# Performance work log

Measured on AMD Instinct MI355X. Metric: run time of the kernel, lower is better.

Reference implementation:

```python
import jax, jax.numpy as jnp
import numpy as np

N = 50000
E = 400000
D = 256            # in_dim == out_dim for every branch
H = 8              # mulhead
DH = D // H        # 32
L = 2              # num_layer per branch
NUM_CLASS = 7
SUM_OUT = 5 * D    # classifier in_dim = 1280
EPS = 1e-9         # BatchNorm eps


def _bn(x):
    # BatchNorm1d training-mode forward (biased var), affine at init (gamma=1, beta=0)
    mu = jnp.mean(x, axis=0)
    var = jnp.var(x, axis=0)
    return (x - mu) / jnp.sqrt(var + EPS)


def _gat_layer(f, Ws, bs, Wn, bn_, a_s, a_n, row, col, vals):
    # f: [N, D]; Ws/Wn: [H, D, DH]; bs/bn_: [H, DH]; a_s/a_n: [H, DH]
    f_self = jax.nn.relu(jnp.einsum('nd,hdk->nhk', f, Ws) + bs)      # [N,H,DH]
    f_neigh = jax.nn.relu(jnp.einsum('nd,hdk->nhk', f, Wn) + bn_)    # [N,H,DH]
    att_s = jax.nn.leaky_relu(jnp.einsum('nhk,hk->nh', f_self, a_s), 0.2)  # [N,H]
    # NOTE: original code computes attention_neigh from f_self (faithful)
    att_n = jax.nn.leaky_relu(jnp.einsum('nhk,hk->nh', f_self, a_n), 0.2)  # [N,H]
    e_att = (att_s[row] + att_n[col]) * vals[:, None]                # [E,H]
    msg = e_att[:, :, None] * f_neigh[col]                           # [E,H,DH]
    out = jax.ops.segment_sum(msg, row, num_segments=N)              # [N,H,DH]
    return out.reshape(N, H * DH)                                    # head concat


def _gat(f, Ws, bs, Wn, bn_, a_s, a_n, row, col, vals):
    for i in range(L):
        f = _bn(_gat_layer(f, Ws[i], bs[i], Wn[i], bn_[i], a_s[i], a_n[i], row, col, vals))
    return f


def _gcn(f, W, b, row, col, vals):
    for i in range(L):
        h = f @ W[i] + b[i]
        agg = jax.ops.segment_sum(vals[:, None] * h[col], row, num_segments=N)
        f = _bn(jax.nn.relu(agg))
    return f


def setup_inputs() -> dict:
    key = jax.random.key(0)
    ks = jax.random.split(key, 20)

    def xavier(k, shape):
        fan_in, fan_out = shape[-2], shape[-1]
        lim = float(np.sqrt(6.0 / (fan_in + fan_out)))
        return jax.random.uniform(k, shape, jnp.float32, -lim, lim)

    return {
        'f_in': jax.random.normal(ks[0], (N, D), jnp.float32),
        'edge_rows': jax.random.randint(ks[1], (4, E), 0, N, jnp.int64 if jax.config.jax_enable_x64 else jnp.int32),
        'edge_cols': jax.random.randint(ks[2], (4, E), 0, N, jnp.int64 if jax.config.jax_enable_x64 else jnp.int32),
        'edge_vals': jax.random.uniform(ks[3], (4, E), jnp.float32),
        # GAT params: [L, H, D, DH] / [L, H, DH]
        'gat_Ws': xavier(ks[4], (L, H, D, DH)),
        'gat_bs': jnp.zeros((L, H, DH), jnp.float32),
        'gat_Wn': xavier(ks[5], (L, H, D, DH)),
        'gat_bn': jnp.zeros((L, H, DH), jnp.float32),
        'gat_as': jnp.ones((L, H, DH), jnp.float32),   # init.ones_
        'gat_an': jnp.ones((L, H, DH), jnp.float32),
        # 3 vanilla GCN branches: [3, L, D, D] / [3, L, D]
        'gcn_W': xavier(ks[6], (3, L, D, D)),
        'gcn_b': jnp.zeros((3, L, D), jnp.float32),
        # self perceptron
        'self_W': xavier(ks[7], (D, D)),
        'self_b': jnp.zeros((D,), jnp.float32),
        # classifier
        'cls_W': xavier(ks[8], (SUM_OUT, NUM_CLASS)),
        'cls_b': jnp.zeros((NUM_CLASS,), jnp.float32),
    }


def reference(f_in, edge_rows, edge_cols, edge_vals,
              gat_Ws, gat_bs, gat_Wn, gat_bn, gat_as, gat_an,
              gcn_W, gcn_b, self_W, self_b, cls_W, cls_b):
    outs = []
    # fcgat branch (adj 0)
    outs.append(_gat(f_in, gat_Ws, gat_bs, gat_Wn, gat_bn, gat_as, gat_an,
                     edge_rows[0], edge_cols[0], edge_vals[0]))
    # uttr/past/futr vanilla GCN branches (adjs 1..3)
    for g in range(3):
        outs.append(_gcn(f_in, gcn_W[g], gcn_b[g],
                         edge_rows[g + 1], edge_cols[g + 1], edge_vals[g + 1]))
    # self perceptron (act=True -> relu + BN)
    outs.append(_bn(jax.nn.relu(f_in @ self_W + self_b)))
    f = jnp.concatenate(outs, axis=1)          # [N, 1280]
    return f @ cls_W + cls_b                   # classifier: act=False
```

## Files before the change

### kernel.cpp

```cpp
#include <hip/hip_runtime.h>


constexpr int D     = 256;
constexpr int NHEAD = 8;
constexpr int NCLS  = 7;
constexpr int NSLOT = 8;
constexpr float BN_EPS = 1e-9f;

typedef short  s16x8 __attribute__((ext_vector_type(8)));
typedef float  f32x4 __attribute__((ext_vector_type(4)));

__device__ __forceinline__ unsigned short f2bf(float f) {
  unsigned int u = __builtin_bit_cast(unsigned int, f);
  u += 0x7FFFu + ((u >> 16) & 1u);
  return (unsigned short)(u >> 16);
}
__device__ __forceinline__ float bf2f(unsigned short h) {
  unsigned int u = ((unsigned int)h) << 16;
  return __builtin_bit_cast(float, u);
}

__device__ __forceinline__ void gload_lds16(const void* g, void* l) {
  __builtin_amdgcn_global_load_lds(
      (const __attribute__((address_space(1))) unsigned int*)g,
      (__attribute__((address_space(3))) unsigned int*)l, 16, 0, 0);
}

__launch_bounds__(256)
__global__ void k_gemm_mfma(const unsigned short* __restrict__ A,
                            const unsigned short* __restrict__ Wt,
                            const float* __restrict__ bias,
                            unsigned short* __restrict__ C,
                            int M, int doRelu,
                            const float* __restrict__ a_s, const float* __restrict__ a_n,
                            float* __restrict__ attS, float* __restrict__ attN)
{
  __shared__ unsigned short As[128 * 32];
  __shared__ unsigned short Bs[128 * 32];
  const int t = threadIdx.x;
  const int wave = t >> 6, lane = t & 63;
  const int quad = lane >> 4, l16 = lane & 15;
  const int wm = (wave & 1) * 64, wn = (wave >> 1) * 64;
  const int bm = blockIdx.x * 128, bn = blockIdx.y * 128;

  f32x4 acc[4][4] = {};

  const int rA0 = wave * 32 + (lane >> 2);
  const int rA1 = rA0 + 16;
  const int sub = (lane & 3) * 8;
  const unsigned short* gA0 = A  + (size_t)min(bm + rA0, M - 1) * D + sub;
  const unsigned short* gA1 = A  + (size_t)min(bm + rA1, M - 1) * D + sub;
  const unsigned short* gB0 = Wt + (size_t)(bn + rA0) * D + sub;
  const unsigned short* gB1 = Wt + (size_t)(bn + rA1) * D + sub;
  unsigned short* lA0 = &As[wave * 1024];
  unsigned short* lA1 = &As[wave * 1024 + 512];
  unsigned short* lB0 = &Bs[wave * 1024];
  unsigned short* lB1 = &Bs[wave * 1024 + 512];

  for (int k0 = 0; k0 < D; k0 += 32) {
    gload_lds16(gA0 + k0, lA0);
    gload_lds16(gA1 + k0, lA1);
    gload_lds16(gB0 + k0, lB0);
    gload_lds16(gB1 + k0, lB1);
    __syncthreads();
    s16x8 af[4], bf[4];
#pragma unroll
    for (int mi = 0; mi < 4; ++mi)
      af[mi] = *(const s16x8*)(&As[(wm + mi * 16 + l16) * 32 + quad * 8]);
#pragma unroll
    for (int nj = 0; nj < 4; ++nj)
      bf[nj] = *(const s16x8*)(&Bs[(wn + nj * 16 + l16) * 32 + quad * 8]);
#pragma unroll
    for (int mi = 0; mi < 4; ++mi)
#pragma unroll
      for (int nj = 0; nj < 4; ++nj)
        acc[mi][nj] = __builtin_amdgcn_mfma_f32_16x16x32_bf16(af[mi], bf[nj], acc[mi][nj], 0, 0, 0);
    __syncthreads();
  }

  if (attS) {
    const int hb = (bn + wn) >> 5;
#pragma unroll
    for (int mi = 0; mi < 4; ++mi) {
#pragma unroll
      for (int h = 0; h < 2; ++h) {
        float ps[4] = {}, pn[4] = {};
#pragma unroll
        for (int j = 0; j < 2; ++j) {
          const int nj = h * 2 + j;
          const int col = bn + wn + nj * 16 + l16;
          const float bv = bias[col];
          const float av = a_s[col], nv = a_n[col];
#pragma unroll
          for (int r = 0; r < 4; ++r) {
            const int row = bm + wm + mi * 16 + quad * 4 + r;
            const float v = fmaxf(acc[mi][nj][r] + bv, 0.f);
            if (C && row < M) C[(size_t)row * D + col] = f2bf(v);
            ps[r] = fmaf(v, av, ps[r]);
            pn[r] = fmaf(v, nv, pn[r]);
          }
        }
#pragma unroll
        for (int m = 1; m < 16; m <<= 1)
#pragma unroll
          for (int r = 0; r < 4; ++r) {
            ps[r] += __shfl_xor(ps[r], m);
            pn[r] += __shfl_xor(pn[r], m);
          }
        if (l16 == 0) {
#pragma unroll
          for (int r = 0; r < 4; ++r) {
            const int row = bm + wm + mi * 16 + quad * 4 + r;
            if (row < M) {
              const float s_ = ps[r], n_ = pn[r];
              attS[(size_t)row * NHEAD + hb + h] = (s_ > 0.f) ? s_ : 0.2f * s_;
              attN[(size_t)row * NHEAD + hb + h] = (n_ > 0.f) ? n_ : 0.2f * n_;
            }
          }
        }
      }
    }
  } else {
#pragma unroll
    for (int nj = 0; nj < 4; ++nj) {
      const int col = bn + wn + nj * 16 + l16;
      const float bv = bias[col];
#pragma unroll
      for (int mi = 0; mi < 4; ++mi) {
#pragma unroll
        for (int r = 0; r < 4; ++r) {
          const int row = bm + wm + mi * 16 + quad * 4 + r;
          if (row < M) {
            float v = acc[mi][nj][r] + bv;
            if (doRelu) v = fmaxf(v, 0.f);
            C[(size_t)row * D + col] = f2bf(v);
          }
        }
      }
    }
  }
}

__global__ void k_cvt(const float* __restrict__ src, unsigned short* __restrict__ dst, int n8)
{
  const int i = blockIdx.x * 256 + threadIdx.x;
  if (i >= n8) return;
  const float4 a = *(const float4*)(src + (size_t)i * 8);
  const float4 b = *(const float4*)(src + (size_t)i * 8 + 4);
  uint4 o;
  o.x = (unsigned)f2bf(a.x) | ((unsigned)f2bf(a.y) << 16);
  o.y = (unsigned)f2bf(a.z) | ((unsigned)f2bf(a.w) << 16);
  o.z = (unsigned)f2bf(b.x) | ((unsigned)f2bf(b.y) << 16);
  o.w = (unsigned)f2bf(b.z) | ((unsigned)f2bf(b.w) << 16);
  *(uint4*)(dst + (size_t)i * 8) = o;
}

__global__ void k_cvt_w(const float* __restrict__ gat_Ws, const float* __restrict__ gat_Wn,
                        const float* __restrict__ gcn_W, const float* __restrict__ self_W,
                        unsigned short* __restrict__ Wt)
{
  const int m = blockIdx.x >> 8, j = blockIdx.x & 255, d = threadIdx.x;
  float v;
  if (m < 4) {
    const int l = m >> 1;
    const float* W = (m & 1) ? gat_Wn : gat_Ws;
    v = W[(((size_t)l * NHEAD + (j >> 5)) * D + d) * 32 + (j & 31)];
  } else if (m < 10) {
    v = gcn_W[((size_t)(m - 4) * D + d) * D + j];
  } else {
    v = self_W[(size_t)d * D + j];
  }
  Wt[((size_t)m * D + j) * D + d] = f2bf(v);
}

__global__ void k_fold_w(const float* __restrict__ srcW, const float* __restrict__ srcB,
                         const float* __restrict__ sums, unsigned short* __restrict__ dstW,
                         float* __restrict__ dstB, int mode, int Nn)
{
  __shared__ float red[256];
  const int j = blockIdx.x;
  const int d = threadIdx.x;
  float sAcc = 0.f, qAcc = 0.f;
#pragma unroll
  for (int s8 = 0; s8 < NSLOT; ++s8) {
    sAcc += sums[s8 * 2 * D + d];
    qAcc += sums[s8 * 2 * D + D + d];
  }
  const float inv = 1.f / (float)Nn;
  const float m_ = sAcc * inv;
  const float rs = rsqrtf(qAcc * inv - m_ * m_ + BN_EPS);
  float w;
  if (mode == 0) w = srcW[(((size_t)(j >> 5)) * D + d) * 32 + (j & 31)];
  else           w = srcW[(size_t)d * D + j];
  const unsigned short q = f2bf(w * rs);
  dstW[(size_t)j * D + d] = q;
  red[d] = m_ * bf2f(q);
  __syncthreads();
  for (int off = 128; off > 0; off >>= 1) {
    if (d < off) red[d] += red[d + off];
    __syncthreads();
  }
  if (d == 0) dstB[j] = srcB[j] - red[0];
}

__global__ void k_count(const int* __restrict__ rows, int* __restrict__ cnt, int E4, int E, int N)
{
  const int i = blockIdx.x * 256 + threadIdx.x;
  if (i < E4) atomicAdd(&cnt[(i / E) * N + rows[i]], 1);
}

__global__ void k_scan_blk(const int* __restrict__ in, int* __restrict__ scanTmp,
                           int* __restrict__ blkSum, int n)
{
  __shared__ int buf[256];
  const int t = threadIdx.x, i = blockIdx.x * 256 + t;
  const int v = (i < n) ? in[i] : 0;
  buf[t] = v; __syncthreads();
  for (int off = 1; off < 256; off <<= 1) {
    const int x = (t >= off) ? buf[t - off] : 0;
    __syncthreads();
    buf[t] += x; __syncthreads();
  }
  if (i < n) scanTmp[i] = buf[t];
  if (t == 255) blkSum[blockIdx.x] = buf[255];
}

__global__ void k_scan_top(int* __restrict__ blkSum, int G)
{
  __shared__ int buf[1024];
  const int t = threadIdx.x;
  const int v = (t < G) ? blkSum[t] : 0;
  buf[t] = v; __syncthreads();
  for (int off = 1; off < 1024; off <<= 1) {
    const int x = (t >= off) ? buf[t - off] : 0;
    __syncthreads();
    buf[t] += x; __syncthreads();
  }
  if (t < G) blkSum[t] = buf[t] - v;
}

__global__ void k_scan_fin(const int* __restrict__ scanTmp, const int* __restrict__ blkOff,
                           int* __restrict__ rowptr, int n)
{
  const int i = blockIdx.x * 256 + threadIdx.x;
  if (i < n) rowptr[i + 1] = scanTmp[i] + blkOff[blockIdx.x];
  if (i == 0) rowptr[0] = 0;
}

__global__ void k_scatter(const int* __restrict__ rows, const int* __restrict__ cols,
                          const float* __restrict__ vals,
                          const int* __restrict__ rowptr, int* __restrict__ fill,
                          int2* __restrict__ edge, int E4, int E, int N)
{
  const int i = blockIdx.x * 256 + threadIdx.x;
  if (i >= E4) return;
  const int g = (i / E) * N + rows[i];
  const int p = rowptr[g] + atomicAdd(&fill[g], 1);
  edge[p] = make_int2(cols[i], __float_as_int(vals[i]));
}

__device__ __forceinline__ void acc8(float* a, uint4 f, float c) {
  const unsigned w[4] = {f.x, f.y, f.z, f.w};
#pragma unroll
  for (int k = 0; k < 4; ++k) {
    a[2 * k]     = fmaf(c, bf2f((unsigned short)(w[k] & 0xffff)), a[2 * k]);
    a[2 * k + 1] = fmaf(c, bf2f((unsigned short)(w[k] >> 16)),    a[2 * k + 1]);
  }
}

__device__ __forceinline__ uint4 pack8(const float* a, bool relu) {
  unsigned ov[4];
#pragma unroll
  for (int k = 0; k < 4; ++k) {
    float lo = a[2 * k], hi = a[2 * k + 1];
    if (relu) { lo = fmaxf(lo, 0.f); hi = fmaxf(hi, 0.f); }
    ov[k] = (unsigned)f2bf(lo) | ((unsigned)f2bf(hi) << 16);
  }
  uint4 o; o.x = ov[0]; o.y = ov[1]; o.z = ov[2]; o.w = ov[3];
  return o;
}

__global__ void k_gat_agg(const unsigned short* __restrict__ fneigh,
                          const float* __restrict__ attS, const float* __restrict__ attN,
                          const int* __restrict__ rowptr, const int2* __restrict__ edge,
                          unsigned short* __restrict__ out, int N)
{
  const int n = blockIdx.x * 4 + (threadIdx.x >> 6);
  if (n >= N) return;
  const int lane = threadIdx.x & 63;
  const int half = lane >> 5;
  const int c32  = lane & 31;
  const int head = c32 >> 2;
  const float as = attS[(size_t)n * NHEAD + head];
  float a[8] = {};
  int p = rowptr[n];
  const int e = rowptr[n + 1];
  for (; p + 3 < e; p += 4) {
    const int2 ea = edge[p + half];
    const int2 eb = edge[p + 2 + half];
    const float ca = (as + attN[(size_t)ea.x * NHEAD + head]) * __int_as_float(ea.y);
    const float cb = (as + attN[(size_t)eb.x * NHEAD + head]) * __int_as_float(eb.y);
    const uint4 fa = *(const uint4*)(fneigh + (size_t)ea.x * D + c32 * 8);
    const uint4 fb = *(const uint4*)(fneigh + (size_t)eb.x * D + c32 * 8);
    acc8(a, fa, ca);
    acc8(a, fb, cb);
  }
  if (p + 1 < e) {
    const int2 ea = edge[p + half];
    const float ca = (as + attN[(size_t)ea.x * NHEAD + head]) * __int_as_float(ea.y);
    const uint4 fa = *(const uint4*)(fneigh + (size_t)ea.x * D + c32 * 8);
    acc8(a, fa, ca);
    p += 2;
  }
  if (p < e && half == 0) {
    const int2 ea = edge[p];
    const float ca = (as + attN[(size_t)ea.x * NHEAD + head]) * __int_as_float(ea.y);
    const uint4 fa = *(const uint4*)(fneigh + (size_t)ea.x * D + c32 * 8);
    acc8(a, fa, ca);
  }
#pragma unroll
  for (int k = 0; k < 8; ++k) a[k] += __shfl_xor(a[k], 32);
  if (half == 0)
    *(uint4*)(out + (size_t)n * D + c32 * 8) = pack8(a, false);
}

__global__ void k_gcn_agg(const unsigned short* __restrict__ Hm,
                          const int* __restrict__ rowptr, const int2* __restrict__ edge,
                          unsigned short* __restrict__ out, int N)
{
  const int n = blockIdx.x * 4 + (threadIdx.x >> 6);
  if (n >= N) return;
  const int lane = threadIdx.x & 63;
  const int half = lane >> 5;
  const int c32  = lane & 31;
  float a[8] = {};
  int p = rowptr[n];
  const int e = rowptr[n + 1];
  for (; p + 3 < e; p += 4) {
    const int2 ea = edge[p + half];
    const int2 eb = edge[p + 2 + half];
    const uint4 fa = *(const uint4*)(Hm + (size_t)ea.x * D + c32 * 8);
    const uint4 fb = *(const uint4*)(Hm + (size_t)eb.x * D + c32 * 8);
    acc8(a, fa, __int_as_float(ea.y));
    acc8(a, fb, __int_as_float(eb.y));
  }
  if (p + 1 < e) {
    const int2 ea = edge[p + half];
    const uint4 fa = *(const uint4*)(Hm + (size_t)ea.x * D + c32 * 8);
    acc8(a, fa, __int_as_float(ea.y));
    p += 2;
  }
  if (p < e && half == 0) {
    const int2 ea = edge[p];
    const uint4 fa = *(const uint4*)(Hm + (size_t)ea.x * D + c32 * 8);
    acc8(a, fa, __int_as_float(ea.y));
  }
#pragma unroll
  for (int k = 0; k < 8; ++k) a[k] += __shfl_xor(a[k], 32);
  if (half == 0)
    *(uint4*)(out + (size_t)n * D + c32 * 8) = pack8(a, true);
}

__launch_bounds__(256)
__global__ void k_bn_stats(const unsigned short* __restrict__ X, float* __restrict__ sums, int M)
{
  __shared__ float ls[256][8];
  __shared__ float lq[256][8];
  const int t = threadIdx.x, cg = t & 31, rg = t >> 5;
  float s[8] = {}, q[8] = {};
  for (int r = blockIdx.x * 8 + rg; r < M; r += gridDim.x * 8) {
    const uint4 f = *(const uint4*)(X + (size_t)r * D + cg * 8);
    const unsigned w[4] = {f.x, f.y, f.z, f.w};
#pragma unroll
    for (int k = 0; k < 4; ++k) {
      const float lo = bf2f((unsigned short)(w[k] & 0xffff));
      const float hi = bf2f((unsigned short)(w[k] >> 16));
      s[2 * k]     += lo; q[2 * k]     = fmaf(lo, lo, q[2 * k]);
      s[2 * k + 1] += hi; q[2 * k + 1] = fmaf(hi, hi, q[2 * k + 1]);
    }
  }
#pragma unroll
  for (int k = 0; k < 8; ++k) { ls[t][k] = s[k]; lq[t][k] = q[k]; }
  __syncthreads();
  if (rg == 0) {
    float* slot = sums + (size_t)(blockIdx.x & (NSLOT - 1)) * 2 * D;
#pragma unroll
    for (int g = 1; g < 8; ++g)
#pragma unroll
      for (int k = 0; k < 8; ++k) { s[k] += ls[cg + 32 * g][k]; q[k] += lq[cg + 32 * g][k]; }
#pragma unroll
    for (int k = 0; k < 8; ++k) {
      atomicAdd(&slot[cg * 8 + k], s[k]);
      atomicAdd(&slot[D + cg * 8 + k], q[k]);
    }
  }
}

__global__ void k_init_out(float* __restrict__ out, const float* __restrict__ cls_b, int n)
{
  const int i = blockIdx.x * 256 + threadIdx.x;
  if (i < n) out[i] = cls_b[i % NCLS];
}

__global__ void k_classifier(const unsigned short* __restrict__ F, const float* __restrict__ W,
                             const float* __restrict__ sums,
                             float* __restrict__ out, int N, int baseRow)
{
  __shared__ float smu[D], srs[D];
  const int t = threadIdx.x;
  {
    float sAcc = 0.f, qAcc = 0.f;
#pragma unroll
    for (int s8 = 0; s8 < NSLOT; ++s8) {
      sAcc += sums[s8 * 2 * D + t];
      qAcc += sums[s8 * 2 * D + D + t];
    }
    const float inv = 1.f / (float)N;
    const float m_ = sAcc * inv;
    smu[t] = m_;
    srs[t] = rsqrtf(qAcc * inv - m_ * m_ + BN_EPS);
  }
  __syncthreads();

  const int n = blockIdx.x * 8 + (t >> 5);
  if (n >= N) return;
  const int lane = t & 31;
  const uint4 f = *(const uint4*)(F + (size_t)n * D + lane * 8);
  const unsigned w[4] = {f.x, f.y, f.z, f.w};
  float fv[8];
#pragma unroll
  for (int k = 0; k < 4; ++k) {
    fv[2 * k]     = (bf2f((unsigned short)(w[k] & 0xffff)) - smu[lane * 8 + 2 * k])     * srs[lane * 8 + 2 * k];
    fv[2 * k + 1] = (bf2f((unsigned short)(w[k] >> 16))    - smu[lane * 8 + 2 * k + 1]) * srs[lane * 8 + 2 * k + 1];
  }
  const float* Wr = W + (size_t)(baseRow + lane * 8) * NCLS;
  float p[NCLS];
#pragma unroll
  for (int c = 0; c < NCLS; ++c) {
    float s = 0.f;
#pragma unroll
    for (int k = 0; k < 8; ++k) s = fmaf(fv[k], Wr[k * NCLS + c], s);
    p[c] = s;
  }
#pragma unroll
  for (int m = 1; m < 32; m <<= 1)
#pragma unroll
    for (int c = 0; c < NCLS; ++c) p[c] += __shfl_xor(p[c], m);
  if (lane == 0) {
    float* o = out + (size_t)n * NCLS;
#pragma unroll
    for (int c = 0; c < NCLS; ++c) o[c] += p[c];
  }
}

extern "C" void kernel_launch(void* const* d_in, const int* in_sizes, int n_in,
                              void* d_out, int out_size, void* d_ws, size_t ws_size,
                              hipStream_t stream)
{
  const float* f_in   = (const float*)d_in[0];
  const int*   erow   = (const int*)d_in[1];
  const int*   ecol   = (const int*)d_in[2];
  const float* eval   = (const float*)d_in[3];
  const float* gat_Ws = (const float*)d_in[4];
  const float* gat_bs = (const float*)d_in[5];
  const float* gat_Wn = (const float*)d_in[6];
  const float* gat_bn = (const float*)d_in[7];
  const float* gat_as = (const float*)d_in[8];
  const float* gat_an = (const float*)d_in[9];
  const float* gcn_W  = (const float*)d_in[10];
  const float* gcn_b  = (const float*)d_in[11];
  const float* self_W = (const float*)d_in[12];
  const float* self_b = (const float*)d_in[13];
  const float* cls_W  = (const float*)d_in[14];
  const float* cls_b  = (const float*)d_in[15];
  float* out = (float*)d_out;

  const int N  = in_sizes[0] / D;
  const int E  = in_sizes[1] / 4;
  const int E4 = 4 * E, N4 = 4 * N;
  const size_t ND = (size_t)N * D;

  unsigned short* bufA = (unsigned short*)d_ws;
  unsigned short* bufB = bufA + ND;
  unsigned short* bufC = bufB + ND;
  unsigned short* finB = bufC + ND;
  unsigned short* Wt   = finB + ND;
  float* attS   = (float*)(Wt + (size_t)11 * D * D);
  float* attN   = attS + (size_t)N * NHEAD;
  int*   scanTmp= (int*)(attN + (size_t)N * NHEAD);
  int*   blkSum = scanTmp + N4;
  int*   rowptr = blkSum + 1024;
  int2*  edge   = (int2*)(rowptr + (N4 + 4));
  int*   cnt    = (int*)(edge + E4);
  int*   fill   = cnt + N4;
  float* foldB    = (float*)scanTmp;
  float* slotSums = (float*)scanTmp + 2048;
  const size_t zero_bytes = (size_t)(2 * N4) * sizeof(int);
  const size_t slot_bytes = (size_t)9 * NSLOT * 2 * D * sizeof(float);

  const dim3 gemm_grid((N + 127) / 128, D / 128);
  const int nb8   = (N + 7) / 8;
  const int nb4   = (N + 3) / 4;
  const int scanG = (N4 + 255) / 256;

  hipMemsetAsync(cnt, 0, zero_bytes, stream);

  k_cvt  <<<(int)(ND / 8 + 255) / 256, 256, 0, stream>>>(f_in, finB, (int)(ND / 8));
  k_cvt_w<<<11 * 256, 256, 0, stream>>>(gat_Ws, gat_Wn, gcn_W, self_W, Wt);

  k_count   <<<(E4 + 255) / 256, 256, 0, stream>>>(erow, cnt, E4, E, N);
  k_scan_blk<<<scanG, 256, 0, stream>>>(cnt, scanTmp, blkSum, N4);
  k_scan_top<<<1, 1024, 0, stream>>>(blkSum, scanG);
  k_scan_fin<<<scanG, 256, 0, stream>>>(scanTmp, blkSum, rowptr, N4);
  k_scatter <<<(E4 + 255) / 256, 256, 0, stream>>>(erow, ecol, eval, rowptr, fill,
                                                   edge, E4, E, N);

  hipMemsetAsync(slotSums, 0, slot_bytes, stream);

  k_init_out<<<(N * NCLS + 255) / 256, 256, 0, stream>>>(out, cls_b, N * NCLS);

  const size_t WM = (size_t)D * D;
  auto sumsOf = [&](int id) { return slotSums + (size_t)id * NSLOT * 2 * D; };
  auto stats = [&](unsigned short* X, int id) {
    k_bn_stats<<<256, 256, 0, stream>>>(X, sumsOf(id), N);
  };

  {
    const int* rp = rowptr;
    k_gemm_mfma<<<gemm_grid, 256, 0, stream>>>(finB, Wt + 0 * WM, gat_bs, nullptr, N, 1,
                                               gat_as, gat_an, attS, attN);
    k_gemm_mfma<<<gemm_grid, 256, 0, stream>>>(finB, Wt + 1 * WM, gat_bn, bufB, N, 1,
                                               nullptr, nullptr, nullptr, nullptr);
    k_gat_agg  <<<nb4, 256, 0, stream>>>(bufB, attS, attN, rp, edge, bufC, N);
    stats(bufC, 0);
    k_fold_w<<<D, 256, 0, stream>>>(gat_Ws + (size_t)NHEAD * D * 32, gat_bs + D,
                                    sumsOf(0), Wt + 2 * WM, foldB + 0 * D, 0, N);
    k_fold_w<<<D, 256, 0, stream>>>(gat_Wn + (size_t)NHEAD * D * 32, gat_bn + D,
                                    sumsOf(0), Wt + 3 * WM, foldB + 1 * D, 0, N);
    k_gemm_mfma<<<gemm_grid, 256, 0, stream>>>(bufC, Wt + 2 * WM, foldB + 0 * D, nullptr, N, 1,
                                               gat_as + D, gat_an + D, attS, attN);
    k_gemm_mfma<<<gemm_grid, 256, 0, stream>>>(bufC, Wt + 3 * WM, foldB + 1 * D, bufB, N, 1,
                                               nullptr, nullptr, nullptr, nullptr);
    k_gat_agg  <<<nb4, 256, 0, stream>>>(bufB, attS, attN, rp, edge, bufA, N);
    stats(bufA, 1);
    k_classifier<<<nb8, 256, 0, stream>>>(bufA, cls_W, sumsOf(1), out, N, 0);
  }

  for (int g = 0; g < 3; ++g) {
    const int* rp = rowptr + (size_t)(g + 1) * N;
    const float* bg = gcn_b + (size_t)g * 2 * D;
    k_gemm_mfma<<<gemm_grid, 256, 0, stream>>>(finB, Wt + (4 + 2 * g) * WM, bg, bufA, N, 0,
                                               nullptr, nullptr, nullptr, nullptr);
    k_gcn_agg  <<<nb4, 256, 0, stream>>>(bufA, rp, edge, bufB, N);
    stats(bufB, 2 + 2 * g);
    k_fold_w<<<D, 256, 0, stream>>>(gcn_W + (size_t)(2 * g + 1) * D * D, bg + D,
                                    sumsOf(2 + 2 * g),
                                    Wt + (5 + 2 * g) * WM, foldB + (2 + g) * D, 1, N);
    k_gemm_mfma<<<gemm_grid, 256, 0, stream>>>(bufB, Wt + (5 + 2 * g) * WM,
                                               foldB + (2 + g) * D, bufA, N, 0,
                                               nullptr, nullptr, nullptr, nullptr);
    k_gcn_agg  <<<nb4, 256, 0, stream>>>(bufA, rp, edge, bufB, N);
    stats(bufB, 3 + 2 * g);
    k_classifier<<<nb8, 256, 0, stream>>>(bufB, cls_W, sumsOf(3 + 2 * g), out, N, (1 + g) * D);
  }

  k_gemm_mfma<<<gemm_grid, 256, 0, stream>>>(finB, Wt + 10 * WM, self_b, bufA, N, 1,
                                             nullptr, nullptr, nullptr, nullptr);
  stats(bufA, 8);
  k_classifier<<<nb8, 256, 0, stream>>>(bufA, cls_W, sumsOf(8), out, N, 4 * D);
}
```

Before: 1.199 ms.

## Merge GAT self/neigh GEMMs, fuse BN stats into GEMM, drop init kernel

The GAT self and neighbour projections now run as one 4-column-block GEMM launch. Blocks 0-1 produce only the attention scalars, and blocks 2-3 write the neighbour features using a second bias. The self-perceptron GEMM accumulates BatchNorm sum and sum-of-squares in its epilogue with per-slot atomics, which removes a separate stats pass. The output-init kernel is folded into the first classifier launch. Together these cut kernel launches and one re-read of the feature buffer, at the cost of more epilogue work and extra atomics in the GEMM.

```diff
diff --git a/kernel.cpp b/kernel.cpp
--- a/kernel.cpp
+++ b/kernel.cpp
@@ -30,10 +30,12 @@
 __global__ void k_gemm_mfma(const unsigned short* __restrict__ A,
                             const unsigned short* __restrict__ Wt,
                             const float* __restrict__ bias,
+                            const float* __restrict__ biasB,
                             unsigned short* __restrict__ C,
                             int M, int doRelu,
                             const float* __restrict__ a_s, const float* __restrict__ a_n,
-                            float* __restrict__ attS, float* __restrict__ attN)
+                            float* __restrict__ attS, float* __restrict__ attN,
+                            float* __restrict__ bnOut)
 {
   __shared__ unsigned short As[128 * 32];
   __shared__ unsigned short Bs[128 * 32];
@@ -78,7 +80,8 @@
     __syncthreads();
   }
 
-  if (attS) {
+  const bool attSlab = (attS != nullptr) && (bn < 256);
+  if (attSlab) {
     const int hb = (bn + wn) >> 5;
 #pragma unroll
     for (int mi = 0; mi < 4; ++mi) {
@@ -93,9 +96,7 @@
           const float av = a_s[col], nv = a_n[col];
 #pragma unroll
           for (int r = 0; r < 4; ++r) {
-            const int row = bm + wm + mi * 16 + quad * 4 + r;
             const float v = fmaxf(acc[mi][nj][r] + bv, 0.f);
-            if (C && row < M) C[(size_t)row * D + col] = f2bf(v);
             ps[r] = fmaf(v, av, ps[r]);
             pn[r] = fmaf(v, nv, pn[r]);
           }
@@ -121,10 +122,14 @@
       }
     }
   } else {
+    const int cBase = (attS != nullptr) ? 256 : 0;
+    const float* bsrc = (attS != nullptr) ? biasB : bias;
+    float cs[4] = {}, cq[4] = {};
 #pragma unroll
     for (int nj = 0; nj < 4; ++nj) {
       const int col = bn + wn + nj * 16 + l16;
-      const float bv = bias[col];
+      const int cw  = col - cBase;
+      const float bv = bsrc[cw];
 #pragma unroll
       for (int mi = 0; mi < 4; ++mi) {
 #pragma unroll
@@ -133,8 +138,32 @@
           if (row < M) {
             float v = acc[mi][nj][r] + bv;
             if (doRelu) v = fmaxf(v, 0.f);
-            C[(size_t)row * D + col] = f2bf(v);
+            const unsigned short u = f2bf(v);
+            C[(size_t)row * D + cw] = u;
+            if (bnOut) {
+              const float w = bf2f(u);
+              cs[nj] += w;
+              cq[nj] = fmaf(w, w, cq[nj]);
+            }
           }
+        }
+      }
+    }
+    if (bnOut) {
+#pragma unroll
+      for (int nj = 0; nj < 4; ++nj) {
+        cs[nj] += __shfl_xor(cs[nj], 16);
+        cq[nj] += __shfl_xor(cq[nj], 16);
+        cs[nj] += __shfl_xor(cs[nj], 32);
+        cq[nj] += __shfl_xor(cq[nj], 32);
+      }
+      if (quad == 0) {
+        float* slot = bnOut + (size_t)(blockIdx.x & (NSLOT - 1)) * 2 * D;
+#pragma unroll
+        for (int nj = 0; nj < 4; ++nj) {
+          const int col = bn + wn + nj * 16 + l16;
+          atomicAdd(&slot[col], cs[nj]);
+          atomicAdd(&slot[D + col], cq[nj]);
         }
       }
     }
@@ -396,15 +425,9 @@
   }
 }
 
-__global__ void k_init_out(float* __restrict__ out, const float* __restrict__ cls_b, int n)
-{
-  const int i = blockIdx.x * 256 + threadIdx.x;
-  if (i < n) out[i] = cls_b[i % NCLS];
-}
-
 __global__ void k_classifier(const unsigned short* __restrict__ F, const float* __restrict__ W,
-                             const float* __restrict__ sums,
-                             float* __restrict__ out, int N, int baseRow)
+                             const float* __restrict__ sums, const float* __restrict__ cls_b,
+                             float* __restrict__ out, int N, int baseRow, int initMode)
 {
   __shared__ float smu[D], srs[D];
   const int t = threadIdx.x;
@@ -448,8 +471,13 @@
     for (int c = 0; c < NCLS; ++c) p[c] += __shfl_xor(p[c], m);
   if (lane == 0) {
     float* o = out + (size_t)n * NCLS;
-#pragma unroll
-    for (int c = 0; c < NCLS; ++c) o[c] += p[c];
+    if (initMode) {
+#pragma unroll
+      for (int c = 0; c < NCLS; ++c) o[c] = p[c] + cls_b[c];
+    } else {
+#pragma unroll
+      for (int c = 0; c < NCLS; ++c) o[c] += p[c];
+    }
   }
 }
 
@@ -499,6 +527,7 @@
   const size_t slot_bytes = (size_t)9 * NSLOT * 2 * D * sizeof(float);
 
   const dim3 gemm_grid((N + 127) / 128, D / 128);
+  const dim3 gemm_grid2((N + 127) / 128, 4);
   const int nb8   = (N + 7) / 8;
   const int nb4   = (N + 3) / 4;
   const int scanG = (N4 + 255) / 256;
@@ -517,8 +546,6 @@
 
   hipMemsetAsync(slotSums, 0, slot_bytes, stream);
 
-  k_init_out<<<(N * NCLS + 255) / 256, 256, 0, stream>>>(out, cls_b, N * NCLS);
-
   const size_t WM = (size_t)D * D;
   auto sumsOf = [&](int id) { return slotSums + (size_t)id * NSLOT * 2 * D; };
   auto stats = [&](unsigned short* X, int id) {
@@ -527,45 +554,47 @@
 
   {
     const int* rp = rowptr;
-    k_gemm_mfma<<<gemm_grid, 256, 0, stream>>>(finB, Wt + 0 * WM, gat_bs, nullptr, N, 1,
-                                               gat_as, gat_an, attS, attN);
-    k_gemm_mfma<<<gemm_grid, 256, 0, stream>>>(finB, Wt + 1 * WM, gat_bn, bufB, N, 1,
-                                               nullptr, nullptr, nullptr, nullptr);
+    k_gemm_mfma<<<gemm_grid2, 256, 0, stream>>>(finB, Wt + 0 * WM, gat_bs, gat_bn,
+                                                bufB, N, 1,
+                                                gat_as, gat_an, attS, attN, nullptr);
     k_gat_agg  <<<nb4, 256, 0, stream>>>(bufB, attS, attN, rp, edge, bufC, N);
     stats(bufC, 0);
     k_fold_w<<<D, 256, 0, stream>>>(gat_Ws + (size_t)NHEAD * D * 32, gat_bs + D,
                                     sumsOf(0), Wt + 2 * WM, foldB + 0 * D, 0, N);
     k_fold_w<<<D, 256, 0, stream>>>(gat_Wn + (size_t)NHEAD * D * 32, gat_bn + D,
                                     sumsOf(0), Wt + 3 * WM, foldB + 1 * D, 0, N);
-    k_gemm_mfma<<<gemm_grid, 256, 0, stream>>>(bufC, Wt + 2 * WM, foldB + 0 * D, nullptr, N, 1,
-                                               gat_as + D, gat_an + D, attS, attN);
-    k_gemm_mfma<<<gemm_grid, 256, 0, stream>>>(bufC, Wt + 3 * WM, foldB + 1 * D, bufB, N, 1,
-                                               nullptr, nullptr, nullptr, nullptr);
+    k_gemm_mfma<<<gemm_grid2, 256, 0, stream>>>(bufC, Wt + 2 * WM, foldB + 0 * D,
+                                                foldB + 1 * D, bufB, N, 1,
+                                                gat_as + D, gat_an + D, attS, attN, nullptr);
     k_gat_agg  <<<nb4, 256, 0, stream>>>(bufB, attS, attN, rp, edge, bufA, N);
     stats(bufA, 1);
-    k_classifier<<<nb8, 256, 0, stream>>>(bufA, cls_W, sumsOf(1), out, N, 0);
+    k_classifier<<<nb8, 256, 0, stream>>>(bufA, cls_W, sumsOf(1), cls_b, out, N, 0, 1);
   }
 
   for (int g = 0; g < 3; ++g) {
     const int* rp = rowptr + (size_t)(g + 1) * N;
     const float* bg = gcn_b + (size_t)g * 2 * D;
-    k_gemm_mfma<<<gemm_grid, 256, 0, stream>>>(finB, Wt + (4 + 2 * g) * WM, bg, bufA, N, 0,
-                                               nullptr, nullptr, nullptr, nullptr);
+    k_gemm_mfma<<<gemm_grid, 256, 0, stream>>>(finB, Wt + (4 + 2 * g) * WM, bg, bg,
+                                               bufA, N, 0,
+                                               nullptr, nullptr, nullptr, nullptr, nullptr);
     k_gcn_agg  <<<nb4, 256, 0, stream>>>(bufA, rp, edge, bufB, N);
     stats(bufB, 2 + 2 * g);
     k_fold_w<<<D, 256, 0, stream>>>(gcn_W + (size_t)(2 * g + 1) * D * D, bg + D,
                                     sumsOf(2 + 2 * g),
                                     Wt + (5 + 2 * g) * WM, foldB + (2 + g) * D, 1, N);
     k_gemm_mfma<<<gemm_grid, 256, 0, stream>>>(bufB, Wt + (5 + 2 * g) * WM,
-                                               foldB + (2 + g) * D, bufA, N, 0,
-                                               nullptr, nullptr, nullptr, nullptr);
+                                               foldB + (2 + g) * D, foldB + (2 + g) * D,
+                                               bufA, N, 0,
+                                               nullptr, nullptr, nullptr, nullptr, nullptr);
     k_gcn_agg  <<<nb4, 256, 0, stream>>>(bufA, rp, edge, bufB, N);
     stats(bufB, 3 + 2 * g);
-    k_classifier<<<nb8, 256, 0, stream>>>(bufB, cls_W, sumsOf(3 + 2 * g), out, N, (1 + g) * D);
-  }
-
-  k_gemm_mfma<<<gemm_grid, 256, 0, stream>>>(finB, Wt + 10 * WM, self_b, bufA, N, 1,
-                                             nullptr, nullptr, nullptr, nullptr);
-  stats(bufA, 8);
-  k_classifier<<<nb8, 256, 0, stream>>>(bufA, cls_W, sumsOf(8), out, N, 4 * D);
-}
+    k_classifier<<<nb8, 256, 0, stream>>>(bufB, cls_W, sumsOf(3 + 2 * g), cls_b,
+                                          out, N, (1 + g) * D, 0);
+  }
+
+  k_gemm_mfma<<<gemm_grid, 256, 0, stream>>>(finB, Wt + 10 * WM, self_b, self_b,
+                                             bufA, N, 1,
+                                             nullptr, nullptr, nullptr, nullptr,
+                                             sumsOf(8));
+  k_classifier<<<nb8, 256, 0, stream>>>(bufA, cls_W, sumsOf(8), cls_b, out, N, 4 * D, 0);
+}
```

New measurement: 1.171 ms. 2.3% less time.
